# Kernel tuning notes

Measured on AMD Instinct MI355X. Metric: run time of the kernel, lower is better.

## Reference

```python
import jax, jax.numpy as jnp
import numpy as np
from jax import lax

V, E, H = 32000, 512, 512
B, S = 64, 64


def _lstm_cell(x, h, c, wih, whh, b):
    # PyTorch gate order: i, f, g, o
    g = x @ wih.T + h @ whh.T + b
    i, f, gg, o = jnp.split(g, 4, axis=-1)
    c2 = jax.nn.sigmoid(f) * c + jax.nn.sigmoid(i) * jnp.tanh(gg)
    h2 = jax.nn.sigmoid(o) * jnp.tanh(c2)
    return h2, c2


def setup_inputs() -> dict:
    key = jax.random.key(0)
    ks = jax.random.split(key, 16)
    s = 0.05
    return {
        "hidden_state": jax.random.normal(ks[0], (4, B, H), jnp.float32) * s,
        "cell_state": jax.random.normal(ks[1], (4, B, H), jnp.float32) * s,
        "Y": jax.random.randint(ks[2], (B, S), 0, V),
        "emb": jax.random.normal(ks[3], (V, E), jnp.float32) * s,
        "w_ih_l0": jax.random.normal(ks[4], (2, 4 * H, E), jnp.float32) * s,
        "w_hh_l0": jax.random.normal(ks[5], (2, 4 * H, H), jnp.float32) * s,
        "b_ih_l0": jax.random.normal(ks[6], (2, 4 * H), jnp.float32) * s,
        "b_hh_l0": jax.random.normal(ks[7], (2, 4 * H), jnp.float32) * s,
        "w_ih_l1": jax.random.normal(ks[8], (2, 4 * H, 2 * H), jnp.float32) * s,
        "w_hh_l1": jax.random.normal(ks[9], (2, 4 * H, H), jnp.float32) * s,
        "b_ih_l1": jax.random.normal(ks[10], (2, 4 * H), jnp.float32) * s,
        "b_hh_l1": jax.random.normal(ks[11], (2, 4 * H), jnp.float32) * s,
        "fc_w": jax.random.normal(ks[12], (V, 2 * H), jnp.float32) * s,
        "fc_b": jax.random.normal(ks[13], (V,), jnp.float32) * s,
    }


def reference(hidden_state, cell_state, Y, emb, w_ih_l0, w_hh_l0, b_ih_l0,
              b_hh_l0, w_ih_l1, w_hh_l1, b_ih_l1, b_hh_l1, fc_w, fc_b):
    # Deterministic teacher-forcing: input at step 0 is Y[:,1]; at step i>0 it is Y[:,i-1].
    idx_seq = jnp.concatenate([Y[:, 1:2], Y[:, :-1]], axis=1)  # (B,S)
    xs = idx_seq.T  # (S,B)
    b0 = b_ih_l0 + b_hh_l0  # (2,4H)
    b1 = b_ih_l1 + b_hh_l1

    def step(carry, idx):
        h, c = carry  # (4,B,H): [l0_fwd, l0_bwd, l1_fwd, l1_bwd]
        x = emb[idx]  # (B,E)
        h0f, c0f = _lstm_cell(x, h[0], c[0], w_ih_l0[0], w_hh_l0[0], b0[0])
        h0b, c0b = _lstm_cell(x, h[1], c[1], w_ih_l0[1], w_hh_l0[1], b0[1])
        x1 = jnp.concatenate([h0f, h0b], axis=-1)  # (B,2H)
        h1f, c1f = _lstm_cell(x1, h[2], c[2], w_ih_l1[0], w_hh_l1[0], b1[0])
        h1b, c1b = _lstm_cell(x1, h[3], c[3], w_ih_l1[1], w_hh_l1[1], b1[1])
        out = jnp.concatenate([h1f, h1b], axis=-1)  # (B,2H)
        h2 = jnp.stack([h0f, h0b, h1f, h1b])
        c2 = jnp.stack([c0f, c0b, c1f, c1b])
        return (h2, c2), out

    (_, _), outs = lax.scan(step, (hidden_state, cell_state), xs)  # (S,B,2H)
    logits = outs @ fc_w.T + fc_b  # (S,B,V)
    # permute to (B,S,V) then flatten, as in the torch code
    return jnp.transpose(logits, (1, 0, 2)).reshape(-1, fc_w.shape[0])
```

## Files before the change

### kernel.cpp

```cpp
#include <hip/hip_runtime.h>
#include <hip/hip_bf16.h>
#include <stdint.h>

#define S_ 64
#define B_ 64
#define E_ 512
#define H_ 512
#define V_ 32000
#define G4 2048
#define SB 4096
#define NG 4096

typedef __attribute__((ext_vector_type(8))) short short8;
typedef __attribute__((ext_vector_type(4))) float f32x4;
typedef __attribute__((ext_vector_type(4))) int i32x4;

static __device__ __forceinline__ unsigned short f2bf(float f) {
  unsigned u = __float_as_uint(f);
  u += 0x7fff + ((u >> 16) & 1);
  return (unsigned short)(u >> 16);
}
static __device__ __forceinline__ float sigm(float x) {
  return 1.f / (1.f + expf(-x));
}

__device__ __forceinline__ void gload_lds16(const void* g, void* l) {
  __builtin_amdgcn_global_load_lds(
      (const __attribute__((address_space(1))) void*)g,
      (__attribute__((address_space(3))) void*)l, 16, 0, 0);
}

__device__ __forceinline__ void st128_sys(void* p, i32x4 v) {
  asm volatile("global_store_dwordx4 %0, %1, off sc0 sc1"
               :: "v"((unsigned long long)p), "v"(v) : "memory");
}
__device__ __forceinline__ void wait_vm0() {
  asm volatile("s_waitcnt vmcnt(0)" ::: "memory");
}

__device__ __forceinline__ void spin_ge(unsigned* c, unsigned tgt) {
  while (__hip_atomic_load(c, __ATOMIC_RELAXED, __HIP_MEMORY_SCOPE_AGENT) < tgt)
    __builtin_amdgcn_s_sleep(1);
}
__device__ __forceinline__ void arrive(unsigned* c) {
  __hip_atomic_fetch_add(c, 1u, __ATOMIC_RELAXED, __HIP_MEMORY_SCOPE_AGENT);
}

#define CIDX(t, d, p) ((((t) * 8) + ((d) * 4) + (p)) * 64)
#define CNT_BYTES (64 * 8 * 64 * 4)

__global__ void k_f2bf(const float* __restrict__ in, unsigned short* __restrict__ out, int n) {
  int i = blockIdx.x * blockDim.x + threadIdx.x;
  int stride = gridDim.x * blockDim.x;
  for (; i < n; i += stride) out[i] = f2bf(in[i]);
}

__global__ void k_addbias(const float* __restrict__ a, const float* __restrict__ b,
                          float* __restrict__ out, int n) {
  int i = blockIdx.x * blockDim.x + threadIdx.x;
  if (i < n) out[i] = a[i] + b[i];
}

__global__ void k_gather(const int* __restrict__ Y, const float* __restrict__ emb,
                         unsigned short* __restrict__ X) {
  int sb = blockIdx.x;
  int t = sb >> 6, b = sb & 63;
  int idx = (t == 0) ? Y[b * S_ + 1] : Y[b * S_ + t - 1];
  const float* src = emb + (size_t)idx * E_;
  unsigned short* dst = X + (size_t)sb * E_;
  for (int e = threadIdx.x; e < E_; e += blockDim.x) dst[e] = f2bf(src[e]);
}

__global__ void k_init_h(const float* __restrict__ hid,
                         unsigned short* __restrict__ h0i, unsigned short* __restrict__ h1i) {
  int i = blockIdx.x * blockDim.x + threadIdx.x;
  if (i >= 4 * B_ * H_) return;
  unsigned short v = f2bf(hid[i]);
  if (i < 2 * B_ * H_) h0i[i] = v;
  else h1i[i - 2 * B_ * H_] = v;
}

template <bool PERMUTE, bool NT>
__global__ __launch_bounds__(256) void k_gemm_nt(
    const unsigned short* __restrict__ A, const unsigned short* __restrict__ B,
    const float* __restrict__ bias, float* __restrict__ C,
    int M, int N, int K, int nTN) {
  __shared__ unsigned short Als[128 * 32];
  __shared__ unsigned short Bls[128 * 32];
  int tid = threadIdx.x;
  int bm = blockIdx.x / nTN, bn = blockIdx.x - bm * nTN;
  int w = tid >> 6, l = tid & 63;
  int wr = w >> 1, wc = w & 1;
  int lr = l & 15, hi = l >> 4;
  int c0 = w * 128 + l;
  int row0 = c0 >> 2, ks0 = (((c0 & 3) ^ (row0 & 3)) * 8);
  int c1 = c0 + 64;
  int row1 = c1 >> 2, ks1 = (((c1 & 3) ^ (row1 & 3)) * 8);
  const unsigned short* Ab = A + (size_t)(bm * 128) * K;
  const unsigned short* Bb = B + (size_t)(bn * 128) * K;
  unsigned short* AlsW = &Als[w * 1024];
  unsigned short* BlsW = &Bls[w * 1024];
  int co = ((hi ^ (lr & 3)) * 8);
  f32x4 acc[4][4] = {};
  for (int kk = 0; kk < K; kk += 32) {
    __syncthreads();
    gload_lds16(Ab + (size_t)row0 * K + kk + ks0, AlsW);
    gload_lds16(Ab + (size_t)row1 * K + kk + ks1, AlsW + 512);
    gload_lds16(Bb + (size_t)row0 * K + kk + ks0, BlsW);
    gload_lds16(Bb + (size_t)row1 * K + kk + ks1, BlsW + 512);
    __syncthreads();
    short8 af[4], bfr[4];
#pragma unroll
    for (int r = 0; r < 4; r++)
      af[r] = *(const short8*)&Als[(wr * 64 + r * 16 + lr) * 32 + co];
#pragma unroll
    for (int c4 = 0; c4 < 4; c4++)
      bfr[c4] = *(const short8*)&Bls[(wc * 64 + c4 * 16 + lr) * 32 + co];
#pragma unroll
    for (int r = 0; r < 4; r++)
#pragma unroll
      for (int c4 = 0; c4 < 4; c4++)
        acc[r][c4] = __builtin_amdgcn_mfma_f32_16x16x32_bf16(af[r], bfr[c4], acc[r][c4], 0, 0, 0);
  }
  int rbase = bm * 128 + wr * 64 + hi * 4;
  int cbase = bn * 128 + wc * 64 + lr;
#pragma unroll
  for (int r = 0; r < 4; r++) {
#pragma unroll
    for (int c4 = 0; c4 < 4; c4++) {
      int cc = cbase + c4 * 16;
      float bv = bias[cc];
#pragma unroll
      for (int j = 0; j < 4; j++) {
        int rr = rbase + r * 16 + j;
        size_t orow = PERMUTE ? (size_t)((rr & 63) * 64 + (rr >> 6)) : (size_t)rr;
        float v = acc[r][c4][j] + bv;
        float* p = &C[orow * (size_t)N + cc];
        if (NT) __builtin_nontemporal_store(v, p);
        else *p = v;
      }
    }
  }
}

#define LDW0 520
#define LDW1 1544
#define NBLK 192

__global__ __launch_bounds__(256) void k_fused_lstm(
    const unsigned short* __restrict__ h0i,
    const unsigned short* __restrict__ h1i,
    const float* __restrict__ cell,
    const unsigned short* __restrict__ whh0,
    const unsigned short* __restrict__ wih1,
    const unsigned short* __restrict__ whh1,
    const float* __restrict__ b1s,
    const float* __restrict__ G0,
    unsigned short* __restrict__ H0,
    unsigned short* __restrict__ O1,
    unsigned* __restrict__ cnt0, unsigned* __restrict__ cnt1) {
  __shared__ unsigned short SM[32 * LDW1];
  __shared__ __align__(16) unsigned short HS[64 * 16];
  int tid = threadIdx.x;
  int w = tid >> 6, l = tid & 63;
  int lr = l & 15, hi = l >> 4;

  if (blockIdx.x < 64) {
    int d = blockIdx.x >> 5, jt = blockIdx.x & 31;
    const unsigned short* Wd = whh0 + (size_t)d * (G4 * H_);
    for (int c = tid; c < 64 * 64; c += 256) {
      int row = c >> 6, ck = c & 63;
      int g = row >> 4, r16 = row & 15;
      *(int4*)&SM[row * LDW0 + ck * 8] =
          *(const int4*)&Wd[(size_t)(g * H_ + jt * 16 + r16) * H_ + ck * 8];
    }
    int j = jt * 16 + lr;
    int b0 = w * 16 + hi * 4;
    f32x4 creg;
    {
      const float* cd = cell + (size_t)d * (B_ * H_);
#pragma unroll
      for (int jj = 0; jj < 4; jj++) creg[jj] = cd[(size_t)(b0 + jj) * H_ + j];
    }
    __syncthreads();
    const float* G_dj = G0 + d * G4;
    float gv[4][4];
    auto preloadG = [&](int t) {
#pragma unroll
      for (int jj = 0; jj < 4; jj++) {
        const float* Gb = G_dj + (size_t)(t * B_ + b0 + jj) * NG;
#pragma unroll
        for (int g = 0; g < 4; g++) gv[g][jj] = Gb[g * 512 + j];
      }
    };
    preloadG(0);
    for (int t = 0; t < S_; ++t) {
      if (t >= 1) {
        if (tid < 4) spin_ge(&cnt0[CIDX(t - 1, d, tid)], 8);
        __syncthreads();
      }
      const unsigned short* hp = (t == 0) ? h0i + (size_t)d * (B_ * H_)
                                          : H0 + (size_t)(t - 1) * B_ * 1024 + d * 512;
      size_t hstr = (t == 0) ? (size_t)H_ : 1024;
      const unsigned short* arow = hp + (size_t)(w * 16 + lr) * hstr + hi * 8;
      f32x4 acc[4] = {};
#pragma unroll
      for (int ki = 0; ki < 16; ki++) {
        short8 a = *(const short8*)&arow[ki * 32];
#pragma unroll
        for (int g = 0; g < 4; g++) {
          short8 bfr = *(const short8*)&SM[(g * 16 + lr) * LDW0 + ki * 32 + hi * 8];
          acc[g] = __builtin_amdgcn_mfma_f32_16x16x32_bf16(a, bfr, acc[g], 0, 0, 0);
        }
      }
#pragma unroll
      for (int jj = 0; jj < 4; jj++) {
        float gi = acc[0][jj] + gv[0][jj];
        float gf = acc[1][jj] + gv[1][jj];
        float gg = acc[2][jj] + gv[2][jj];
        float go = acc[3][jj] + gv[3][jj];
        float c = sigm(gf) * creg[jj] + sigm(gi) * tanhf(gg);
        creg[jj] = c;
        HS[(b0 + jj) * 16 + lr] = f2bf(sigm(go) * tanhf(c));
      }
      __syncthreads();
      unsigned short* Ho = H0 + (size_t)t * B_ * 1024 + d * 512 + jt * 16;
      if (tid < 128) {
        int r = tid >> 1, half = tid & 1;
        i32x4 v = *(const i32x4*)&HS[r * 16 + half * 8];
        st128_sys(&Ho[(size_t)r * 1024 + half * 8], v);
      }
      wait_vm0();
      __syncthreads();
      if (tid == 0) arrive(&cnt0[CIDX(t, d, jt & 3)]);
      if (t + 1 < S_) preloadG(t + 1);
    }
  } else {
    int idx = blockIdx.x - 64;
    int d = idx >> 6, jt8 = idx & 63;
    int j0 = jt8 * 8;
    {
      const unsigned short* Wih = wih1 + (size_t)d * (G4 * 1024);
      const unsigned short* Whh = whh1 + (size_t)d * (G4 * H_);
      for (int c = tid; c < 32 * 192; c += 256) {
        int r = c / 192, ck = c - r * 192;
        int g = r >> 3, jc = r & 7;
        const unsigned short* src =
            (ck < 128) ? Wih + (size_t)(g * H_ + j0 + jc) * 1024 + ck * 8
                       : Whh + (size_t)(g * H_ + j0 + jc) * H_ + (ck - 128) * 8;
        *(int4*)&SM[r * LDW1 + ck * 8] = *(const int4*)src;
      }
    }
    int j = j0 + (lr & 7);
    const float* b1d = b1s + d * G4;
    float bi_ = b1d[j], bf_ = b1d[512 + j], bg_ = b1d[1024 + j], bo_ = b1d[1536 + j];
    int b0 = w * 16 + hi * 4;
    f32x4 creg = {};
    if (lr < 8) {
      const float* cd = cell + (size_t)(2 + d) * (B_ * H_);
#pragma unroll
      for (int jj = 0; jj < 4; jj++) creg[jj] = cd[(size_t)(b0 + jj) * H_ + j];
    }
    __syncthreads();
    for (int t = 0; t < S_; ++t) {
      if (tid < 8) spin_ge(&cnt0[CIDX(t, 0, 0) + tid * 64], 8);
      if (t >= 1 && tid >= 8 && tid < 12) spin_ge(&cnt1[CIDX(t - 1, d, tid - 8)], 16);
      __syncthreads();
      const unsigned short* x1row = H0 + ((size_t)t * B_ + w * 16 + lr) * 1024 + hi * 8;
      const unsigned short* hprev = (t == 0)
          ? h1i + (size_t)d * (B_ * H_) + (size_t)(w * 16 + lr) * H_ + hi * 8
          : O1 + ((size_t)(t - 1) * B_ + w * 16 + lr) * 1024 + d * 512 + hi * 8;
      f32x4 acc0 = {}, acc1 = {};
#pragma unroll 8
      for (int ki = 0; ki < 32; ki++) {
        short8 a = *(const short8*)&x1row[ki * 32];
        short8 bA = *(const short8*)&SM[(size_t)lr * LDW1 + ki * 32 + hi * 8];
        short8 bB = *(const short8*)&SM[(size_t)(16 + lr) * LDW1 + ki * 32 + hi * 8];
        acc0 = __builtin_amdgcn_mfma_f32_16x16x32_bf16(a, bA, acc0, 0, 0, 0);
        acc1 = __builtin_amdgcn_mfma_f32_16x16x32_bf16(a, bB, acc1, 0, 0, 0);
      }
#pragma unroll 8
      for (int ki = 0; ki < 16; ki++) {
        short8 a = *(const short8*)&hprev[ki * 32];
        short8 bA = *(const short8*)&SM[(size_t)lr * LDW1 + 1024 + ki * 32 + hi * 8];
        short8 bB = *(const short8*)&SM[(size_t)(16 + lr) * LDW1 + 1024 + ki * 32 + hi * 8];
        acc0 = __builtin_amdgcn_mfma_f32_16x16x32_bf16(a, bA, acc0, 0, 0, 0);
        acc1 = __builtin_amdgcn_mfma_f32_16x16x32_bf16(a, bB, acc1, 0, 0, 0);
      }
      float pf[4], po[4];
#pragma unroll
      for (int jj = 0; jj < 4; jj++) {
        pf[jj] = __shfl_xor(acc0[jj], 8);
        po[jj] = __shfl_xor(acc1[jj], 8);
      }
      if (lr < 8) {
#pragma unroll
        for (int jj = 0; jj < 4; jj++) {
          float gi = acc0[jj] + bi_;
          float gf = pf[jj] + bf_;
          float gg = acc1[jj] + bg_;
          float go = po[jj] + bo_;
          float c = sigm(gf) * creg[jj] + sigm(gi) * tanhf(gg);
          creg[jj] = c;
          HS[(b0 + jj) * 8 + lr] = f2bf(sigm(go) * tanhf(c));
        }
      }
      __syncthreads();
      unsigned short* Oo = O1 + (size_t)t * B_ * 1024 + d * 512 + j0;
      if (tid < 64) {
        i32x4 v = *(const i32x4*)&HS[tid * 8];
        st128_sys(&Oo[(size_t)tid * 1024], v);
      }
      wait_vm0();
      __syncthreads();
      if (tid == 0 && t + 1 < S_) arrive(&cnt1[CIDX(t, d, jt8 & 3)]);
    }
  }
}

extern "C" void kernel_launch(void* const* d_in, const int* in_sizes, int n_in,
                              void* d_out, int out_size, void* d_ws, size_t ws_size,
                              hipStream_t stream) {
  const float* hidden = (const float*)d_in[0];
  const float* cell   = (const float*)d_in[1];
  const int*   Y      = (const int*)d_in[2];
  const float* emb    = (const float*)d_in[3];
  const float* wih0   = (const float*)d_in[4];
  const float* whh0   = (const float*)d_in[5];
  const float* bih0   = (const float*)d_in[6];
  const float* bhh0   = (const float*)d_in[7];
  const float* wih1   = (const float*)d_in[8];
  const float* whh1   = (const float*)d_in[9];
  const float* bih1   = (const float*)d_in[10];
  const float* bhh1   = (const float*)d_in[11];
  const float* fcw    = (const float*)d_in[12];
  const float* fcb    = (const float*)d_in[13];

  char* ws = (char*)d_ws;
  size_t off = 0;
  auto alloc = [&](size_t bytes) {
    void* p = ws + off;
    off += (bytes + 255) & ~(size_t)255;
    return p;
  };
  unsigned short* wih0b = (unsigned short*)alloc((size_t)2 * G4 * E_ * 2);
  unsigned short* whh0b = (unsigned short*)alloc((size_t)2 * G4 * H_ * 2);
  unsigned short* wih1b = (unsigned short*)alloc((size_t)2 * G4 * 1024 * 2);
  unsigned short* whh1b = (unsigned short*)alloc((size_t)2 * G4 * H_ * 2);
  unsigned short* fcwb  = (unsigned short*)alloc((size_t)V_ * 1024 * 2);
  unsigned short* Xb    = (unsigned short*)alloc((size_t)SB * E_ * 2);
  unsigned short* H0    = (unsigned short*)alloc((size_t)SB * 1024 * 2);
  unsigned short* O1    = (unsigned short*)alloc((size_t)SB * 1024 * 2);
  unsigned short* h0i   = (unsigned short*)alloc((size_t)2 * B_ * H_ * 2);
  unsigned short* h1i   = (unsigned short*)alloc((size_t)2 * B_ * H_ * 2);
  float* b0s = (float*)alloc((size_t)2 * G4 * 4);
  float* b1s = (float*)alloc((size_t)2 * G4 * 4);
  unsigned* cnt0 = (unsigned*)alloc(CNT_BYTES);
  unsigned* cnt1 = (unsigned*)alloc(CNT_BYTES);
  (void)ws_size;

  float* G0 = (float*)d_out;

  k_f2bf<<<2048, 256, 0, stream>>>(wih0, wih0b, 2 * G4 * E_);
  k_f2bf<<<2048, 256, 0, stream>>>(whh0, whh0b, 2 * G4 * H_);
  k_f2bf<<<2048, 256, 0, stream>>>(wih1, wih1b, 2 * G4 * 1024);
  k_f2bf<<<2048, 256, 0, stream>>>(whh1, whh1b, 2 * G4 * H_);
  k_f2bf<<<4096, 256, 0, stream>>>(fcw, fcwb, V_ * 1024);
  k_addbias<<<16, 256, 0, stream>>>(bih0, bhh0, b0s, 2 * G4);
  k_addbias<<<16, 256, 0, stream>>>(bih1, bhh1, b1s, 2 * G4);
  k_gather<<<SB, 256, 0, stream>>>(Y, emb, Xb);
  k_init_h<<<512, 256, 0, stream>>>(hidden, h0i, h1i);
  (void)hipMemsetAsync(cnt0, 0, CNT_BYTES, stream);
  (void)hipMemsetAsync(cnt1, 0, CNT_BYTES, stream);

  k_gemm_nt<false, false><<<(SB / 128) * (NG / 128), 256, 0, stream>>>(
      Xb, wih0b, b0s, G0, SB, NG, E_, NG / 128);

  k_fused_lstm<<<NBLK, 256, 0, stream>>>(h0i, h1i, cell, whh0b, wih1b, whh1b,
                                         b1s, G0, H0, O1, cnt0, cnt1);

  k_gemm_nt<true, true><<<(SB / 128) * (V_ / 128), 256, 0, stream>>>(
      O1, fcwb, fcb, (float*)d_out, SB, V_, 1024, V_ / 128);
}
```

Measured before the change: 1.235 ms.

## Prefetch layer-1 input projection ahead of recurrence and remap GEMM workgroups per XCD

In the fused LSTM kernel, the layer-1 input-projection MFMA for step t+1 now runs right after step t's output is published, before waiting on the recurrent dependency. This takes that work off the serial critical path, so each step only waits for the h_prev contribution. Separately, the GEMM block index is remapped so consecutive blocks on the same XCD share column tiles (M-major ordering with an 8-way swizzle), which should improve L2 reuse. The swizzle assumes nwg is divisible by 8, and the reordered spins change the synchronisation structure.

```diff
diff --git a/kernel.cpp b/kernel.cpp
--- a/kernel.cpp
+++ b/kernel.cpp
@@ -84,11 +84,13 @@
 __global__ __launch_bounds__(256) void k_gemm_nt(
     const unsigned short* __restrict__ A, const unsigned short* __restrict__ B,
     const float* __restrict__ bias, float* __restrict__ C,
-    int M, int N, int K, int nTN) {
+    int M, int N, int K, int nTM, int nwg) {
   __shared__ unsigned short Als[128 * 32];
   __shared__ unsigned short Bls[128 * 32];
   int tid = threadIdx.x;
-  int bm = blockIdx.x / nTN, bn = blockIdx.x - bm * nTN;
+  int o = blockIdx.x;
+  int wg = (o & 7) * (nwg >> 3) + (o >> 3);
+  int bm = wg % nTM, bn = wg / nTM;
   int w = tid >> 6, l = tid & 63;
   int wr = w >> 1, wc = w & 1;
   int lr = l & 15, hi = l >> 4;
@@ -262,15 +264,13 @@
       for (int jj = 0; jj < 4; jj++) creg[jj] = cd[(size_t)(b0 + jj) * H_ + j];
     }
     __syncthreads();
-    for (int t = 0; t < S_; ++t) {
-      if (tid < 8) spin_ge(&cnt0[CIDX(t, 0, 0) + tid * 64], 8);
-      if (t >= 1 && tid >= 8 && tid < 12) spin_ge(&cnt1[CIDX(t - 1, d, tid - 8)], 16);
+
+    f32x4 acc0, acc1;
+    {
+      if (tid < 8) spin_ge(&cnt0[CIDX(0, 0, 0) + tid * 64], 8);
       __syncthreads();
-      const unsigned short* x1row = H0 + ((size_t)t * B_ + w * 16 + lr) * 1024 + hi * 8;
-      const unsigned short* hprev = (t == 0)
-          ? h1i + (size_t)d * (B_ * H_) + (size_t)(w * 16 + lr) * H_ + hi * 8
-          : O1 + ((size_t)(t - 1) * B_ + w * 16 + lr) * 1024 + d * 512 + hi * 8;
-      f32x4 acc0 = {}, acc1 = {};
+      acc0 = {}; acc1 = {};
+      const unsigned short* x1row = H0 + ((size_t)0 * B_ + w * 16 + lr) * 1024 + hi * 8;
 #pragma unroll 8
       for (int ki = 0; ki < 32; ki++) {
         short8 a = *(const short8*)&x1row[ki * 32];
@@ -279,6 +279,15 @@
         acc0 = __builtin_amdgcn_mfma_f32_16x16x32_bf16(a, bA, acc0, 0, 0, 0);
         acc1 = __builtin_amdgcn_mfma_f32_16x16x32_bf16(a, bB, acc1, 0, 0, 0);
       }
+    }
+    for (int t = 0; t < S_; ++t) {
+      if (t >= 1) {
+        if (tid < 4) spin_ge(&cnt1[CIDX(t - 1, d, tid)], 16);
+        __syncthreads();
+      }
+      const unsigned short* hprev = (t == 0)
+          ? h1i + (size_t)d * (B_ * H_) + (size_t)(w * 16 + lr) * H_ + hi * 8
+          : O1 + ((size_t)(t - 1) * B_ + w * 16 + lr) * 1024 + d * 512 + hi * 8;
 #pragma unroll 8
       for (int ki = 0; ki < 16; ki++) {
         short8 a = *(const short8*)&hprev[ki * 32];
@@ -314,6 +323,21 @@
       wait_vm0();
       __syncthreads();
       if (tid == 0 && t + 1 < S_) arrive(&cnt1[CIDX(t, d, jt8 & 3)]);
+      if (t + 1 < S_) {
+        if (tid < 8) spin_ge(&cnt0[CIDX(t + 1, 0, 0) + tid * 64], 8);
+        __syncthreads();
+        acc0 = {}; acc1 = {};
+        const unsigned short* x1row =
+            H0 + ((size_t)(t + 1) * B_ + w * 16 + lr) * 1024 + hi * 8;
+#pragma unroll 8
+        for (int ki = 0; ki < 32; ki++) {
+          short8 a = *(const short8*)&x1row[ki * 32];
+          short8 bA = *(const short8*)&SM[(size_t)lr * LDW1 + ki * 32 + hi * 8];
+          short8 bB = *(const short8*)&SM[(size_t)(16 + lr) * LDW1 + ki * 32 + hi * 8];
+          acc0 = __builtin_amdgcn_mfma_f32_16x16x32_bf16(a, bA, acc0, 0, 0, 0);
+          acc1 = __builtin_amdgcn_mfma_f32_16x16x32_bf16(a, bB, acc1, 0, 0, 0);
+        }
+      }
     }
   }
 }
@@ -374,11 +398,11 @@
   (void)hipMemsetAsync(cnt1, 0, CNT_BYTES, stream);
 
   k_gemm_nt<false, false><<<(SB / 128) * (NG / 128), 256, 0, stream>>>(
-      Xb, wih0b, b0s, G0, SB, NG, E_, NG / 128);
+      Xb, wih0b, b0s, G0, SB, NG, E_, SB / 128, (SB / 128) * (NG / 128));
 
   k_fused_lstm<<<NBLK, 256, 0, stream>>>(h0i, h1i, cell, whh0b, wih1b, whh1b,
                                          b1s, G0, H0, O1, cnt0, cnt1);
 
   k_gemm_nt<true, true><<<(SB / 128) * (V_ / 128), 256, 0, stream>>>(
-      O1, fcwb, fcb, (float*)d_out, SB, V_, 1024, V_ / 128);
-}
+      O1, fcwb, fcb, (float*)d_out, SB, V_, 1024, SB / 128, (SB / 128) * (V_ / 128));
+}
```

New measurement: 1.205 ms. 2.4% less time.
